# Kernel optimization log

Measured on AMD Instinct MI355X. Metric: run time of the kernel, lower is better.

## Reference

```python
import jax, jax.numpy as jnp
import numpy as np

HEADS = 4
DIM_HEAD = 32


def setup_inputs() -> dict:
    key = jax.random.key(0)
    k1, k2, k3, k4 = jax.random.split(key, 4)
    dim = 64
    hidden = HEADS * DIM_HEAD  # 128
    x = jax.random.normal(k1, (1, dim, 16, 16, 16), jnp.float32)
    # Conv3d 1x1 kernels collapse to [out_ch, in_ch] matrices
    w_qkv = jax.random.normal(k2, (hidden * 3, dim), jnp.float32) * 0.05
    w_out = jax.random.normal(k3, (dim, hidden), jnp.float32) * 0.05
    b_out = jax.random.normal(k4, (dim,), jnp.float32) * 0.05
    return {"x": x, "w_qkv": w_qkv, "w_out": w_out, "b_out": b_out}


def reference(x, w_qkv, w_out, b_out):
    scale = DIM_HEAD ** -0.5
    b, c, dz, dy, dx = x.shape
    n = dz * dy * dx
    xf = x.reshape(b, c, n)  # flatten spatial dims
    # 1x1 Conv3d (no bias) == channel matmul: [b, 3*hidden, n]
    qkv = jnp.einsum('oc,bcn->bon', w_qkv, xf)
    q, k, v = jnp.split(qkv, 3, axis=1)  # each [b, hidden, n]
    def split_heads(t):
        return t.reshape(b, HEADS, DIM_HEAD, n)  # [b, h, d, n]
    q, k, v = split_heads(q), split_heads(k), split_heads(v)
    q = q * scale
    # sim[b,h,i,j] = sum_d q[b,h,d,i] k[b,h,d,j]
    sim = jnp.einsum('bhdi,bhdj->bhij', q, k)
    sim = sim - jax.lax.stop_gradient(jnp.max(sim, axis=-1, keepdims=True))
    attn = jax.nn.softmax(sim, axis=-1)
    # out[b,h,i,d] = sum_j attn[b,h,i,j] v[b,h,d,j]
    out = jnp.einsum('bhij,bhdj->bhid', attn, v)
    # 'b h (z y x) d -> b (h d) z y x'
    out = out.transpose(0, 1, 3, 2).reshape(b, HEADS * DIM_HEAD, n)
    # final 1x1 Conv3d with bias
    y = jnp.einsum('oc,bcn->bon', w_out, out) + b_out[None, :, None]
    return y.reshape(b, -1, dz, dy, dx)
```

## Files before the change

kernel.cpp:

```cpp
#include <hip/hip_runtime.h>


typedef _Float16 f16x8 __attribute__((ext_vector_type(8)));
typedef _Float16 f16x4 __attribute__((ext_vector_type(4)));
typedef _Float16 f16x2v __attribute__((ext_vector_type(2)));
typedef float f32x4 __attribute__((ext_vector_type(4)));

static __device__ inline f16x4 pack4(float a, float b, float c, float d) {
  f16x4 r;
  r.x = (_Float16)a; r.y = (_Float16)b; r.z = (_Float16)c; r.w = (_Float16)d;
  return r;
}
static __device__ inline f16x2v pack2(float a, float b) {
  f16x2v r;
  r.x = (_Float16)a; r.y = (_Float16)b;
  return r;
}

__global__ __launch_bounds__(256) void qkv_kernel(
    const float* __restrict__ x, const float* __restrict__ w,
    _Float16* __restrict__ qo, _Float16* __restrict__ ko, _Float16* __restrict__ vo)
{
  __shared__ __align__(16) float xs[64 * 68];
  __shared__ __align__(16) float wsb[32 * 68];
  const int t = threadIdx.x;
  const int n0 = blockIdx.x * 64;
  const int o0 = blockIdx.y * 32;
  #pragma unroll
  for (int i = 0; i < 4; ++i) {
    int ch = t + i * 256;
    int c = ch >> 4, p = ch & 15;
    *reinterpret_cast<float4*>(&xs[c * 68 + p * 4]) =
        *reinterpret_cast<const float4*>(&x[c * 4096 + n0 + p * 4]);
  }
  #pragma unroll
  for (int i = 0; i < 2; ++i) {
    int ch = t + i * 256;
    int o = ch >> 4, p = ch & 15;
    *reinterpret_cast<float4*>(&wsb[o * 68 + p * 4]) =
        *reinterpret_cast<const float4*>(&w[(o0 + o) * 64 + p * 4]);
  }
  __syncthreads();
  const int oL = (t >> 5) * 4;
  const int nL = (t & 31) * 2;
  float acc[4][2] = {};
  for (int c4 = 0; c4 < 64; c4 += 4) {
    float2 xa[4];
    #pragma unroll
    for (int k = 0; k < 4; ++k)
      xa[k] = *reinterpret_cast<const float2*>(&xs[(c4 + k) * 68 + nL]);
    #pragma unroll
    for (int i = 0; i < 4; ++i) {
      float4 wv = *reinterpret_cast<const float4*>(&wsb[(oL + i) * 68 + c4]);
      acc[i][0] += wv.x * xa[0].x + wv.y * xa[1].x + wv.z * xa[2].x + wv.w * xa[3].x;
      acc[i][1] += wv.x * xa[0].y + wv.y * xa[1].y + wv.z * xa[2].y + wv.w * xa[3].y;
    }
  }
  const float qs = 0.17677669529663689f * 1.4426950408889634f;
  if (o0 < 128) {
    int ho = o0 >> 5;
    #pragma unroll
    for (int j = 0; j < 2; ++j) {
      int n = n0 + nL + j;
      *reinterpret_cast<f16x4*>(&qo[(ho * 4096 + n) * 32 + oL]) =
          pack4(acc[0][j] * qs, acc[1][j] * qs, acc[2][j] * qs, acc[3][j] * qs);
    }
  } else if (o0 < 256) {
    int ho = (o0 - 128) >> 5;
    #pragma unroll
    for (int j = 0; j < 2; ++j) {
      int n = n0 + nL + j;
      *reinterpret_cast<f16x4*>(&ko[(ho * 4096 + n) * 32 + oL]) =
          pack4(acc[0][j], acc[1][j], acc[2][j], acc[3][j]);
    }
  } else {
    #pragma unroll
    for (int i = 0; i < 4; ++i) {
      *reinterpret_cast<f16x2v*>(&vo[(size_t)(o0 - 256 + oL + i) * 4096 + n0 + nL]) =
          pack2(acc[i][0], acc[i][1]);
    }
  }
}

__global__ __launch_bounds__(256, 4) void attn_kernel(
    const _Float16* __restrict__ qg, const _Float16* __restrict__ kg,
    const _Float16* __restrict__ vg, float* __restrict__ Opart,
    float* __restrict__ lpart, int jlen)
{
  __shared__ __align__(16) _Float16 Ks[2][64 * 40];
  __shared__ __align__(16) _Float16 Vs[2][32 * 72];
  const int t = threadIdx.x;
  const int ck = blockIdx.x;
  const int qt = blockIdx.y;
  const int h  = blockIdx.z;
  const int w = t >> 6;
  const int lane = t & 63;
  const int m = lane & 15;
  const int quad = lane >> 4;
  const int qw = qt * 128 + w * 32;

  f16x8 aq[2];
  #pragma unroll
  for (int g = 0; g < 2; ++g)
    aq[g] = *reinterpret_cast<const f16x8*>(
        &qg[(h * 4096 + qw + g * 16 + m) * 32 + quad * 8]);

  f32x4 acc[2][2];
  #pragma unroll
  for (int g = 0; g < 2; ++g) {
    acc[g][0] = f32x4{0.f, 0.f, 0.f, 0.f};
    acc[g][1] = f32x4{0.f, 0.f, 0.f, 0.f};
  }
  float ls[2] = {0.f, 0.f};

  const int jbeg = ck * jlen;
  const int kr = t >> 2, ksg = t & 3;
  const int vr = t >> 3, vsg = t & 7;
  const _Float16* kgp = kg + (size_t)(h * 4096 + jbeg + kr) * 32 + ksg * 8;
  const _Float16* vgp = vg + (size_t)(h * 32 + vr) * 4096 + jbeg + vsg * 8;

  *reinterpret_cast<uint4*>(&Ks[0][kr * 40 + ksg * 8]) =
      *reinterpret_cast<const uint4*>(kgp);
  *reinterpret_cast<uint4*>(&Vs[0][vr * 72 + vsg * 8]) =
      *reinterpret_cast<const uint4*>(vgp);
  __syncthreads();

  for (int it = 0; it < jlen; it += 64) {
    const int buf = (it >> 6) & 1;
    if (it + 64 < jlen) {
      *reinterpret_cast<uint4*>(&Ks[buf ^ 1][kr * 40 + ksg * 8]) =
          *reinterpret_cast<const uint4*>(kgp + (size_t)(it + 64) * 32);
      *reinterpret_cast<uint4*>(&Vs[buf ^ 1][vr * 72 + vsg * 8]) =
          *reinterpret_cast<const uint4*>(vgp + it + 64);
    }
    #pragma unroll
    for (int jt = 0; jt < 4; ++jt) {
      f16x8 kf = *reinterpret_cast<const f16x8*>(&Ks[buf][(jt * 16 + m) * 40 + quad * 8]);
      f16x4 vf0 = *reinterpret_cast<const f16x4*>(&Vs[buf][m * 72 + jt * 16 + quad * 4]);
      f16x4 vf1 = *reinterpret_cast<const f16x4*>(&Vs[buf][(16 + m) * 72 + jt * 16 + quad * 4]);
      f32x4 z = {0.f, 0.f, 0.f, 0.f};
      f32x4 sT[2];
      #pragma unroll
      for (int g = 0; g < 2; ++g)
        sT[g] = __builtin_amdgcn_mfma_f32_16x16x32_f16(kf, aq[g], z, 0, 0, 0);
      #pragma unroll
      for (int g = 0; g < 2; ++g) {
        float p0 = exp2f(sT[g][0]), p1 = exp2f(sT[g][1]);
        float p2 = exp2f(sT[g][2]), p3 = exp2f(sT[g][3]);
        ls[g] += (p0 + p1) + (p2 + p3);
        f16x4 p = pack4(p0, p1, p2, p3);
        acc[g][0] = __builtin_amdgcn_mfma_f32_16x16x16f16(p, vf0, acc[g][0], 0, 0, 0);
        acc[g][1] = __builtin_amdgcn_mfma_f32_16x16x16f16(p, vf1, acc[g][1], 0, 0, 0);
      }
    }
    __syncthreads();
  }

  #pragma unroll
  for (int g = 0; g < 2; ++g) {
    ls[g] += __shfl_xor(ls[g], 16);
    ls[g] += __shfl_xor(ls[g], 32);
  }
  const size_t cb = (size_t)(ck * 4 + h) * 4096;
  #pragma unroll
  for (int g = 0; g < 2; ++g) {
    #pragma unroll
    for (int dt = 0; dt < 2; ++dt) {
      #pragma unroll
      for (int r = 0; r < 4; ++r) {
        int q = qw + g * 16 + quad * 4 + r;
        Opart[(cb + q) * 32 + dt * 16 + m] = acc[g][dt][r];
      }
    }
  }
  if (quad == 0) {
    #pragma unroll
    for (int g = 0; g < 2; ++g)
      lpart[cb + qw + g * 16 + m] = ls[g];
  }
}

__global__ __launch_bounds__(256) void out_kernel(
    const float* __restrict__ Opart, const float* __restrict__ lpart,
    const float* __restrict__ wo, const float* __restrict__ bo,
    float* __restrict__ y)
{
  __shared__ __align__(16) float as[16 * 132];
  __shared__ __align__(16) float wsh[64 * 132];
  __shared__ float linv[64];
  const int t = threadIdx.x;
  const int nb = blockIdx.x * 16;
  if (t < 64) {
    int h = t >> 4, r = t & 15;
    float s = 0.f;
    #pragma unroll
    for (int ck = 0; ck < 8; ++ck)
      s += lpart[(size_t)(ck * 4 + h) * 4096 + nb + r];
    linv[t] = 1.f / s;
  }
  {
    int ch = t;
    #pragma unroll
    for (int i = 0; i < 8; ++i, ch += 256) {
      int r = ch >> 5, p = ch & 31;
      *reinterpret_cast<float4*>(&wsh[r * 132 + p * 4]) =
          *reinterpret_cast<const float4*>(&wo[r * 128 + p * 4]);
    }
  }
  __syncthreads();
  {
    int ch = t;
    #pragma unroll
    for (int i = 0; i < 2; ++i, ch += 256) {
      int r = ch >> 5, p = ch & 31;
      int h = p >> 3, d4 = (p & 7) * 4;
      float4 s = {0.f, 0.f, 0.f, 0.f};
      #pragma unroll
      for (int ck = 0; ck < 8; ++ck) {
        float4 o4 = *reinterpret_cast<const float4*>(
            &Opart[((size_t)(ck * 4 + h) * 4096 + nb + r) * 32 + d4]);
        s.x += o4.x; s.y += o4.y; s.z += o4.z; s.w += o4.w;
      }
      float inv = linv[h * 16 + r];
      s.x *= inv; s.y *= inv; s.z *= inv; s.w *= inv;
      *reinterpret_cast<float4*>(&as[r * 132 + p * 4]) = s;
    }
  }
  __syncthreads();
  const int oL = (t >> 4) * 4;
  const int n = t & 15;
  float acc[4] = {0.f, 0.f, 0.f, 0.f};
  for (int c = 0; c < 128; c += 4) {
    float4 a = *reinterpret_cast<const float4*>(&as[n * 132 + c]);
    #pragma unroll
    for (int i = 0; i < 4; ++i) {
      float4 wv = *reinterpret_cast<const float4*>(&wsh[(oL + i) * 132 + c]);
      acc[i] += wv.x * a.x + wv.y * a.y + wv.z * a.z + wv.w * a.w;
    }
  }
  #pragma unroll
  for (int i = 0; i < 4; ++i) {
    y[(size_t)(oL + i) * 4096 + nb + n] = acc[i] + bo[oL + i];
  }
}

extern "C" void kernel_launch(void* const* d_in, const int* in_sizes, int n_in,
                              void* d_out, int out_size, void* d_ws, size_t ws_size,
                              hipStream_t stream) {
  (void)in_sizes; (void)n_in; (void)out_size; (void)ws_size;
  const float* x     = (const float*)d_in[0];
  const float* w_qkv = (const float*)d_in[1];
  const float* w_out = (const float*)d_in[2];
  const float* b_out = (const float*)d_in[3];
  float* y = (float*)d_out;
  _Float16* qb = (_Float16*)d_ws;
  _Float16* kb = qb + 524288;
  _Float16* vb = kb + 524288;
  float* Opart = (float*)(vb + 524288);
  float* lpart = Opart + 4194304;

  qkv_kernel<<<dim3(64, 12), 256, 0, stream>>>(x, w_qkv, qb, kb, vb);
  attn_kernel<<<dim3(8, 32, 4), 256, 0, stream>>>(qb, kb, vb, Opart, lpart, 4096 / 8);
  out_kernel<<<256, 256, 0, stream>>>(Opart, lpart, w_out, b_out, y);
}
```

Measured before the change: 103.1 us.

## Double attention block to 512 threads, sharing K/V tiles across eight waves

The attention kernel now runs 512 threads per block, covering 256 queries, so each K/V tile staged in shared memory is reused by twice as many query waves and the grid halves. The copy work is split so the first 256 threads load K and the other 256 load V, with one 16-byte load each instead of two. The output kernel also moves to 512 threads, each handling two output channels and one reduction chunk. The larger blocks cut redundant global K/V traffic but may lower occupancy, since launch bounds of 512 with 4 blocks per unit tighten register limits, and fewer blocks are launched.

```diff
diff --git a/kernel.cpp b/kernel.cpp
--- a/kernel.cpp
+++ b/kernel.cpp
@@ -82,7 +82,7 @@
   }
 }
 
-__global__ __launch_bounds__(256, 4) void attn_kernel(
+__global__ __launch_bounds__(512, 4) void attn_kernel(
     const _Float16* __restrict__ qg, const _Float16* __restrict__ kg,
     const _Float16* __restrict__ vg, float* __restrict__ Opart,
     float* __restrict__ lpart, int jlen)
@@ -97,7 +97,7 @@
   const int lane = t & 63;
   const int m = lane & 15;
   const int quad = lane >> 4;
-  const int qw = qt * 128 + w * 32;
+  const int qw = qt * 256 + w * 32;
 
   f16x8 aq[2];
   #pragma unroll
@@ -114,24 +114,34 @@
   float ls[2] = {0.f, 0.f};
 
   const int jbeg = ck * jlen;
-  const int kr = t >> 2, ksg = t & 3;
-  const int vr = t >> 3, vsg = t & 7;
-  const _Float16* kgp = kg + (size_t)(h * 4096 + jbeg + kr) * 32 + ksg * 8;
-  const _Float16* vgp = vg + (size_t)(h * 32 + vr) * 4096 + jbeg + vsg * 8;
-
-  *reinterpret_cast<uint4*>(&Ks[0][kr * 40 + ksg * 8]) =
-      *reinterpret_cast<const uint4*>(kgp);
-  *reinterpret_cast<uint4*>(&Vs[0][vr * 72 + vsg * 8]) =
-      *reinterpret_cast<const uint4*>(vgp);
+  const bool isK = (t < 256);
+  const _Float16* gp;
+  int ldsoff;
+  if (isK) {
+    int kr = t >> 2, ksg = t & 3;
+    gp = kg + (size_t)(h * 4096 + jbeg + kr) * 32 + ksg * 8;
+    ldsoff = kr * 40 + ksg * 8;
+  } else {
+    int c = t - 256, vr = c >> 3, vsg = c & 7;
+    gp = vg + (size_t)(h * 32 + vr) * 4096 + jbeg + vsg * 8;
+    ldsoff = vr * 72 + vsg * 8;
+  }
+
+  if (isK)
+    *reinterpret_cast<uint4*>(&Ks[0][ldsoff]) = *reinterpret_cast<const uint4*>(gp);
+  else
+    *reinterpret_cast<uint4*>(&Vs[0][ldsoff]) = *reinterpret_cast<const uint4*>(gp);
   __syncthreads();
 
   for (int it = 0; it < jlen; it += 64) {
     const int buf = (it >> 6) & 1;
     if (it + 64 < jlen) {
-      *reinterpret_cast<uint4*>(&Ks[buf ^ 1][kr * 40 + ksg * 8]) =
-          *reinterpret_cast<const uint4*>(kgp + (size_t)(it + 64) * 32);
-      *reinterpret_cast<uint4*>(&Vs[buf ^ 1][vr * 72 + vsg * 8]) =
-          *reinterpret_cast<const uint4*>(vgp + it + 64);
+      if (isK)
+        *reinterpret_cast<uint4*>(&Ks[buf ^ 1][ldsoff]) =
+            *reinterpret_cast<const uint4*>(gp + (size_t)(it + 64) * 32);
+      else
+        *reinterpret_cast<uint4*>(&Vs[buf ^ 1][ldsoff]) =
+            *reinterpret_cast<const uint4*>(gp + (it + 64));
     }
     #pragma unroll
     for (int jt = 0; jt < 4; ++jt) {
@@ -180,7 +190,7 @@
   }
 }
 
-__global__ __launch_bounds__(256) void out_kernel(
+__global__ __launch_bounds__(512) void out_kernel(
     const float* __restrict__ Opart, const float* __restrict__ lpart,
     const float* __restrict__ wo, const float* __restrict__ bo,
     float* __restrict__ y)
@@ -201,7 +211,7 @@
   {
     int ch = t;
     #pragma unroll
-    for (int i = 0; i < 8; ++i, ch += 256) {
+    for (int i = 0; i < 4; ++i, ch += 512) {
       int r = ch >> 5, p = ch & 31;
       *reinterpret_cast<float4*>(&wsh[r * 132 + p * 4]) =
           *reinterpret_cast<const float4*>(&wo[r * 128 + p * 4]);
@@ -209,37 +219,33 @@
   }
   __syncthreads();
   {
-    int ch = t;
-    #pragma unroll
-    for (int i = 0; i < 2; ++i, ch += 256) {
-      int r = ch >> 5, p = ch & 31;
-      int h = p >> 3, d4 = (p & 7) * 4;
-      float4 s = {0.f, 0.f, 0.f, 0.f};
-      #pragma unroll
-      for (int ck = 0; ck < 8; ++ck) {
-        float4 o4 = *reinterpret_cast<const float4*>(
-            &Opart[((size_t)(ck * 4 + h) * 4096 + nb + r) * 32 + d4]);
-        s.x += o4.x; s.y += o4.y; s.z += o4.z; s.w += o4.w;
-      }
-      float inv = linv[h * 16 + r];
-      s.x *= inv; s.y *= inv; s.z *= inv; s.w *= inv;
-      *reinterpret_cast<float4*>(&as[r * 132 + p * 4]) = s;
-    }
-  }
-  __syncthreads();
-  const int oL = (t >> 4) * 4;
+    int r = t >> 5, p = t & 31;
+    int h = p >> 3, d4 = (p & 7) * 4;
+    float4 s = {0.f, 0.f, 0.f, 0.f};
+    #pragma unroll
+    for (int ck = 0; ck < 8; ++ck) {
+      float4 o4 = *reinterpret_cast<const float4*>(
+          &Opart[((size_t)(ck * 4 + h) * 4096 + nb + r) * 32 + d4]);
+      s.x += o4.x; s.y += o4.y; s.z += o4.z; s.w += o4.w;
+    }
+    float inv = linv[h * 16 + r];
+    s.x *= inv; s.y *= inv; s.z *= inv; s.w *= inv;
+    *reinterpret_cast<float4*>(&as[r * 132 + p * 4]) = s;
+  }
+  __syncthreads();
+  const int oL = (t >> 4) * 2;
   const int n = t & 15;
-  float acc[4] = {0.f, 0.f, 0.f, 0.f};
+  float acc[2] = {0.f, 0.f};
   for (int c = 0; c < 128; c += 4) {
     float4 a = *reinterpret_cast<const float4*>(&as[n * 132 + c]);
     #pragma unroll
-    for (int i = 0; i < 4; ++i) {
+    for (int i = 0; i < 2; ++i) {
       float4 wv = *reinterpret_cast<const float4*>(&wsh[(oL + i) * 132 + c]);
       acc[i] += wv.x * a.x + wv.y * a.y + wv.z * a.z + wv.w * a.w;
     }
   }
   #pragma unroll
-  for (int i = 0; i < 4; ++i) {
+  for (int i = 0; i < 2; ++i) {
     y[(size_t)(oL + i) * 4096 + nb + n] = acc[i] + bo[oL + i];
   }
 }
@@ -260,6 +266,6 @@
   float* lpart = Opart + 4194304;
 
   qkv_kernel<<<dim3(64, 12), 256, 0, stream>>>(x, w_qkv, qb, kb, vb);
-  attn_kernel<<<dim3(8, 32, 4), 256, 0, stream>>>(qb, kb, vb, Opart, lpart, 4096 / 8);
-  out_kernel<<<256, 256, 0, stream>>>(Opart, lpart, w_out, b_out, y);
-}
+  attn_kernel<<<dim3(8, 16, 4), 512, 0, stream>>>(qb, kb, vb, Opart, lpart, 4096 / 8);
+  out_kernel<<<256, 512, 0, stream>>>(Opart, lpart, w_out, b_out, y);
+}
```

Result: no change. 103.0 us (-0.0%).
